# Performance work log

Hardware: AMD Instinct MI355X
Metric: run time of the kernel (lower is better)

## Reference

```python
import jax, jax.numpy as jnp
import numpy as np

K = 3        # kernel
S = 2        # downsample scale
P = 1        # padding
C = 96       # input channels
G = C // 6   # groups = 16 (use_group=True)
BN_EPS = 1e-5


def setup_inputs() -> dict:
    key = jax.random.key(0)
    k1, k2, k3, k4, k5 = jax.random.split(key, 5)
    b, h, w = 4, 256, 512
    x = jax.random.normal(k1, (b, C, h, w), dtype=jnp.float32)
    # convbn: Conv2d(C, C*S, k=3, stride=2, pad=1, bias=False) + BatchNorm2d(C*S)
    w1 = jax.random.normal(k2, (C * S, C, K, K), dtype=jnp.float32) * 0.05
    gamma = jax.random.uniform(k3, (C * S,), dtype=jnp.float32, minval=0.5, maxval=1.5)
    beta = jax.random.normal(k4, (C * S,), dtype=jnp.float32) * 0.1
    # 1x1 conv: C*S -> G * K^2, bias=False
    w2 = jax.random.normal(k5, (G * K * K, C * S, 1, 1), dtype=jnp.float32) * 0.05
    return {"x": x, "w1": w1, "gamma": gamma, "beta": beta, "w2": w2}


def _conv(x, w, stride, pad):
    return jax.lax.conv_general_dilated(
        x, w, window_strides=(stride, stride), padding=[(pad, pad), (pad, pad)],
        dimension_numbers=("NCHW", "OIHW", "NCHW"))


def _unfold_patches(x):
    # F.unfold(x, [K,K], stride=S, padding=P) viewed as (b, c, K*K, h', w')
    b, c, h, w = x.shape
    ho, wo = h // S, w // S
    xp = jnp.pad(x, ((0, 0), (0, 0), (P, P), (P, P)))
    taps = [xp[:, :, i:i + ho * S:S, j:j + wo * S:S] for i in range(K) for j in range(K)]
    return jnp.stack(taps, axis=2)  # (b, c, K^2, h', w')


def reference(x, w1, gamma, beta, w2):
    b, c, h, w = x.shape
    ho, wo = h // S, w // S
    # conv_mask branch: conv -> BN (eval: mean=0, var=1) -> LeakyReLU(0.1) -> 1x1 conv
    y = _conv(x, w1, S, P)
    y = y * (gamma / jnp.sqrt(1.0 + BN_EPS))[None, :, None, None] + beta[None, :, None, None]
    y = jnp.where(y >= 0, y, 0.1 * y)
    mask = _conv(y, w2, 1, 0)                                  # (b, G*K^2, h', w')
    mask = mask.reshape(b, 1, G, K * K, ho, wo)
    mask = jax.nn.softmax(mask, axis=3)
    # unfold and group split: channel index = i*G + g  (torch view semantics)
    patches = _unfold_patches(x)                               # (b, c, K^2, h', w')
    patches = patches.reshape(b, c // G, G, K * K, ho, wo)
    out = jnp.sum(mask * patches, axis=3)                      # (b, c//G, G, h', w')
    return out.reshape(b, c, ho, wo)
```

## Files before the change

kernel.cpp:

```cpp
#include <hip/hip_runtime.h>
#include <hip/hip_bf16.h>

#define Bb 4
#define Cc 96
#define Hh 256
#define Ww 512
#define OC 192
#define HO 128
#define WO 256
#define Gg 16
#define CPG 6

typedef __attribute__((ext_vector_type(4))) float f32x4;
typedef __attribute__((ext_vector_type(8))) short bf16x8;
typedef __attribute__((ext_vector_type(4))) short bf16x4;

static __device__ __forceinline__ ushort f2b(float f) {
    __hip_bfloat16 h = __float2bfloat16(f);
    return *reinterpret_cast<ushort*>(&h);
}
static __device__ __forceinline__ float b2f(ushort u) {
    unsigned int v = ((unsigned int)u) << 16;
    return __builtin_bit_cast(float, v);
}

__global__ __launch_bounds__(64) void pack_w1(const float* __restrict__ w1,
                                              ushort* __restrict__ apack) {
    const int blk = blockIdx.x;
    const int k0 = blk / 12;
    const int mf = blk % 12;
    const int lane = threadIdx.x;
    const int m = mf * 16 + (lane & 15);
    const int chunk = k0 / 9;
    const int tap = k0 % 9;
    ushort* dst = apack + (((size_t)(k0 * 12 + mf) * 64) + lane) * 8;
#pragma unroll
    for (int j = 0; j < 8; ++j) {
        const int klocal = ((lane >> 4) << 3) + j;
        const int ic = chunk * 32 + klocal;
        dst[j] = f2b(w1[(size_t)(m * Cc + ic) * 9 + tap]);
    }
}

__global__ __launch_bounds__(64) void pack_w2(const float* __restrict__ w2,
                                              ushort* __restrict__ w2p) {
    const int blk = blockIdx.x;
    const int ks = blk / 9;
    const int mf = blk % 9;
    const int lane = threadIdx.x;
    const int X = lane & 15;
    const int qq = X >> 2;
    const int rr = X & 3;
    const int s = mf * 4 + rr;
    const int g = qq * 4 + s / 9;
    const int k = s % 9;
    const int m = g * 9 + k;
    ushort* dst = w2p + (((size_t)(ks * 9 + mf) * 64) + lane) * 8;
#pragma unroll
    for (int j = 0; j < 8; ++j) {
        const int klocal = ((lane >> 4) << 3) + j;
        const int c = ks * 32 + klocal;
        dst[j] = f2b(w2[(size_t)m * OC + c]);
    }
}

#define XL_MAIN (6 * 4 * 128 * 8)
#define UNION_USHORTS (XL_MAIN + 3 * 32)

__global__ __launch_bounds__(512) void fused(
        const float* __restrict__ x, const ushort* __restrict__ apack,
        const ushort* __restrict__ w2p,
        const float* __restrict__ gamma, const float* __restrict__ beta,
        float* __restrict__ out) {
    __shared__ __align__(16) ushort smem[UNION_USHORTS];
    __shared__ float sc[OC], bi[OC];

    const int bid0 = blockIdx.x;
    const int bid = (bid0 & 7) * 128 + (bid0 >> 3);
    const int owt = bid & 1;
    const int oh = (bid >> 1) & 127;
    const int b = bid >> 8;
    const int ow0 = owt * 128;
    const int tid = threadIdx.x;
    const int wid = tid >> 6;
    const int wm = wid & 1;
    const int wn = wid >> 1;
    const int lane = tid & 63;
    const int r = lane & 15;
    const int q = lane >> 4;

    if (tid < OC) {
        const float bnr = 1.0f / sqrtf(1.0f + 1e-5f);
        sc[tid] = gamma[tid] * bnr;
        bi[tid] = beta[tid];
    }

    f32x4 cacc[6][2];
#pragma unroll
    for (int mf = 0; mf < 6; ++mf)
#pragma unroll
        for (int nf = 0; nf < 2; ++nf) cacc[mf][nf] = (f32x4){0.f, 0.f, 0.f, 0.f};

    const size_t chs = (size_t)Hh * Ww;

    for (int chunk = 0; chunk < 3; ++chunk) {
        __syncthreads();
        const int icc = chunk * 32;
#pragma unroll
        for (int it = 0; it < 3; ++it) {
            const int g2 = tid + (it << 9);
            const int oct = g2 & 3;
            const int colp = (g2 >> 2) & 127;
            const int row = g2 >> 9;
            const int ih = 2 * oh - 1 + row;
            const int gcol = 2 * ow0 + 2 * colp;
            float2 v[8];
            if (ih >= 0) {
                const float* xp = x + ((size_t)(b * Cc + icc + (oct << 3)) * Hh + ih) * Ww + gcol;
#pragma unroll
                for (int j = 0; j < 8; ++j)
                    v[j] = *reinterpret_cast<const float2*>(xp + (size_t)j * chs);
            } else {
#pragma unroll
                for (int j = 0; j < 8; ++j) v[j] = make_float2(0.f, 0.f);
            }
            bf16x8 u0, u1;
#pragma unroll
            for (int j = 0; j < 8; ++j) {
                u0[j] = (short)f2b(v[j].x);
                u1[j] = (short)f2b(v[j].y);
            }
            *reinterpret_cast<bf16x8*>(smem + (((row * 2 + 0) * 4 + oct) * 128 + colp) * 8) = u0;
            *reinterpret_cast<bf16x8*>(smem + (((row * 2 + 1) * 4 + oct) * 128 + colp) * 8) = u1;
        }
        if (tid < 12) {
            const int oct = tid & 3;
            const int row = tid >> 2;
            const int ih = 2 * oh - 1 + row;
            const int gcol = 2 * ow0 - 1;
            float v[8];
            if (ih >= 0 && gcol >= 0) {
                const float* xp = x + ((size_t)(b * Cc + icc + (oct << 3)) * Hh + ih) * Ww + gcol;
#pragma unroll
                for (int j = 0; j < 8; ++j) v[j] = xp[(size_t)j * chs];
            } else {
#pragma unroll
                for (int j = 0; j < 8; ++j) v[j] = 0.f;
            }
            bf16x8 u;
#pragma unroll
            for (int j = 0; j < 8; ++j) u[j] = (short)f2b(v[j]);
            *reinterpret_cast<bf16x8*>(smem + XL_MAIN + row * 32 + oct * 8) = u;
        }
        __syncthreads();

#pragma unroll
        for (int tap = 0; tap < 9; ++tap) {
            const int kh = tap / 3, kw = tap % 3;
            const int par = (kw == 1) ? 0 : 1;
            const int cb = (kw == 0) ? -1 : 0;
            const int k0 = chunk * 9 + tap;

            bf16x8 af[6];
            const ushort* ap = apack + (((size_t)(k0 * 12 + wm * 6) * 64) + lane) * 8;
#pragma unroll
            for (int mf = 0; mf < 6; ++mf)
                af[mf] = *reinterpret_cast<const bf16x8*>(ap + (size_t)mf * 64 * 8);

            bf16x8 bfr[2];
#pragma unroll
            for (int nf = 0; nf < 2; ++nf) {
                const int n = wn * 32 + nf * 16 + r;
                const int colc = n + cb;
                const ushort* src = (colc >= 0)
                    ? smem + (((kh * 2 + par) * 4 + q) * 128 + colc) * 8
                    : smem + XL_MAIN + kh * 32 + q * 8;
                bfr[nf] = *reinterpret_cast<const bf16x8*>(src);
            }
#pragma unroll
            for (int mf = 0; mf < 6; ++mf)
#pragma unroll
                for (int nf = 0; nf < 2; ++nf)
                    cacc[mf][nf] = __builtin_amdgcn_mfma_f32_16x16x32_bf16(
                        af[mf], bfr[nf], cacc[mf][nf], 0, 0, 0);
        }
    }

    __syncthreads();
#pragma unroll
    for (int mf = 0; mf < 6; ++mf) {
        const int cbase = wm * 96 + mf * 16;
        const int coct = (cbase >> 3) + (q >> 1);
#pragma unroll
        for (int nf = 0; nf < 2; ++nf) {
            const int ow = wn * 32 + nf * 16 + r;
            ushort pk[4];
#pragma unroll
            for (int rr = 0; rr < 4; ++rr) {
                const int oc = cbase + q * 4 + rr;
                float v = cacc[mf][nf][rr] * sc[oc] + bi[oc];
                v = (v >= 0.f) ? v : 0.1f * v;
                pk[rr] = f2b(v);
            }
            *reinterpret_cast<bf16x4*>(smem + (coct * 128 + ow) * 8 + (q & 1) * 4) =
                *reinterpret_cast<bf16x4*>(pk);
        }
    }
    __syncthreads();

    const int hi = wid >> 2;
    const int mfbase = hi * 4;
    f32x4 macc[5];
#pragma unroll
    for (int mf = 0; mf < 5; ++mf) macc[mf] = (f32x4){0.f, 0.f, 0.f, 0.f};

    const int owq = (wid & 3) * 32 + (q >> 1) * 16 + r;
    const int owq9 = (wid & 3) * 16 + r + ((wid >> 2) ? 0 : 0);
    (void)owq9;
#pragma unroll
    for (int ks = 0; ks < 6; ++ks) {
        bf16x8 af[5];
        const ushort* ap = w2p + (((size_t)(ks * 9 + mfbase) * 64) + lane) * 8;
#pragma unroll
        for (int mf = 0; mf < 5; ++mf)
            af[mf] = *reinterpret_cast<const bf16x8*>(ap + (size_t)mf * 64 * 8);
        bf16x8 bfr0 = *reinterpret_cast<const bf16x8*>(
            smem + ((ks * 4 + q) * 128 + (wid & 3) * 32 + 0 * 16 + r) * 8);
        bf16x8 bfr1 = *reinterpret_cast<const bf16x8*>(
            smem + ((ks * 4 + q) * 128 + (wid & 3) * 32 + 1 * 16 + r) * 8);
#pragma unroll
        for (int mf = 0; mf < 5; ++mf) {
            macc[mf] = __builtin_amdgcn_mfma_f32_16x16x32_bf16(af[mf], bfr0, macc[mf], 0, 0, 0);
        }
        (void)bfr1;
    }
    f32x4 macc2[5];
#pragma unroll
    for (int mf = 0; mf < 5; ++mf) macc2[mf] = (f32x4){0.f, 0.f, 0.f, 0.f};
#pragma unroll
    for (int ks = 0; ks < 6; ++ks) {
        bf16x8 af[5];
        const ushort* ap = w2p + (((size_t)(ks * 9 + mfbase) * 64) + lane) * 8;
#pragma unroll
        for (int mf = 0; mf < 5; ++mf)
            af[mf] = *reinterpret_cast<const bf16x8*>(ap + (size_t)mf * 64 * 8);
        bf16x8 bfr = *reinterpret_cast<const bf16x8*>(
            smem + ((ks * 4 + q) * 128 + (wid & 3) * 32 + 16 + r) * 8);
#pragma unroll
        for (int mf = 0; mf < 5; ++mf)
            macc2[mf] = __builtin_amdgcn_mfma_f32_16x16x32_bf16(af[mf], bfr, macc2[mf], 0, 0, 0);
    }
    __syncthreads();

#pragma unroll
    for (int nf = 0; nf < 2; ++nf) {
        const int ow = (wid & 3) * 32 + nf * 16 + r;
        const int col = (ow + q * 16) & 127;
#pragma unroll
        for (int gi = 0; gi < 2; ++gi) {
            const int gl = (wid >> 2) * 2 + gi;
            const int g = q * 4 + gl;
            float pv[9];
            float mx = -1e30f;
#pragma unroll
            for (int k = 0; k < 9; ++k) {
                const int s = gl * 9 + k;
                const int mi = (s >> 2) - ((wid >> 2) ? 4 : 0);
                pv[k] = 0.f; (void)mi;
            }
            (void)pv; (void)mx; (void)g; (void)col;
        }
        break;
    }
    {
        if (hi == 0) {
#pragma unroll
            for (int nf = 0; nf < 2; ++nf) {
                const int ow = (wid & 3) * 32 + nf * 16 + r;
                const int col = (ow + q * 16) & 127;
                const f32x4(&mc)[5] = (nf == 0) ? macc : macc2;
#pragma unroll
                for (int gi = 0; gi < 2; ++gi) {
                    const int gl = gi;
                    const int g = q * 4 + gl;
                    float pv[9]; float mx = -1e30f;
#pragma unroll
                    for (int k = 0; k < 9; ++k) {
                        const int s = gl * 9 + k;
                        pv[k] = mc[s >> 2][s & 3];
                        mx = fmaxf(mx, pv[k]);
                    }
                    float ssum = 0.f;
#pragma unroll
                    for (int k = 0; k < 9; ++k) { pv[k] = __expf(pv[k] - mx); ssum += pv[k]; }
                    const float inv = 1.f / ssum;
#pragma unroll
                    for (int k = 0; k < 9; ++k)
                        smem[(g * 9 + k) * 128 + col] = f2b(pv[k] * inv);
                }
            }
        } else {
#pragma unroll
            for (int nf = 0; nf < 2; ++nf) {
                const int ow = (wid & 3) * 32 + nf * 16 + r;
                const int col = (ow + q * 16) & 127;
                const f32x4(&mc)[5] = (nf == 0) ? macc : macc2;
#pragma unroll
                for (int gi = 0; gi < 2; ++gi) {
                    const int gl = 2 + gi;
                    const int g = q * 4 + gl;
                    float pv[9]; float mx = -1e30f;
#pragma unroll
                    for (int k = 0; k < 9; ++k) {
                        const int s = gl * 9 + k;
                        pv[k] = mc[(s >> 2) - 4][s & 3];
                        mx = fmaxf(mx, pv[k]);
                    }
                    float ssum = 0.f;
#pragma unroll
                    for (int k = 0; k < 9; ++k) { pv[k] = __expf(pv[k] - mx); ssum += pv[k]; }
                    const float inv = 1.f / ssum;
#pragma unroll
                    for (int k = 0; k < 9; ++k)
                        smem[(g * 9 + k) * 128 + col] = f2b(pv[k] * inv);
                }
            }
        }
    }
    __syncthreads();

    const int ih0 = 2 * oh - 1;
    const bool okh0 = (oh > 0);
#pragma unroll
    for (int it = 0; it < 4; ++it) {
        const int idx = (it << 9) + tid;
        const int g = idx >> 7;
        const int owl = idx & 127;
        const int owg = ow0 + owl;
        const int col = (owl + (g >> 2) * 16) & 127;

        float p[9];
#pragma unroll
        for (int k = 0; k < 9; ++k) p[k] = b2f(smem[(g * 9 + k) * 128 + col]);

        const int iw0 = 2 * owg - 1;
        const bool okw0 = (owg > 0);
#pragma unroll
        for (int i = 0; i < CPG; ++i) {
            const int cc = i * Gg + g;
            const float* xc = x + (size_t)(b * Cc + cc) * chs;
            float acc = 0.f;
#pragma unroll
            for (int kh = 0; kh < 3; ++kh) {
                if (kh == 0 && !okh0) continue;
                const float* rowp = xc + (size_t)(ih0 + kh) * Ww + iw0;
                const float v0 = okw0 ? rowp[0] : 0.f;
                const float2 v12 = *reinterpret_cast<const float2*>(rowp + 1);
                acc += p[kh * 3 + 0] * v0 + p[kh * 3 + 1] * v12.x
                     + p[kh * 3 + 2] * v12.y;
            }
            out[((size_t)(b * Cc + cc) * HO + oh) * WO + owg] = acc;
        }
    }
}

extern "C" void kernel_launch(void* const* d_in, const int* in_sizes, int n_in,
                              void* d_out, int out_size, void* d_ws, size_t ws_size,
                              hipStream_t stream) {
    const float* x     = (const float*)d_in[0];
    const float* w1    = (const float*)d_in[1];
    const float* gamma = (const float*)d_in[2];
    const float* beta  = (const float*)d_in[3];
    const float* w2    = (const float*)d_in[4];
    float* out = (float*)d_out;

    ushort* apack = (ushort*)d_ws;
    ushort* w2p   = (ushort*)((char*)d_ws + 331776);

    pack_w1<<<27 * 12, 64, 0, stream>>>(w1, apack);
    pack_w2<<<6 * 9, 64, 0, stream>>>(w2, w2p);
    fused<<<Bb * HO * 2, 512, 0, stream>>>(x, apack, w2p, gamma, beta, out);
}
```

Baseline: 174.6 us.

## Prefetch next input-channel chunk into registers during MFMA compute

Global loads of the next 32-channel input chunk are issued into registers right after the LDS barrier, so they overlap the conv MFMA taps of the current chunk instead of stalling at the start of each chunk. The two separate 1x1-conv MFMA loops are also merged so the w2 fragments are loaded once per k-step and feed both column halves. Launch bounds now request 4 blocks per CU. The extra prefetch registers (about 56 floats per thread) plus a tighter register cap could cause spills or reduce overlap.

```diff
diff --git a/kernel.cpp b/kernel.cpp
--- a/kernel.cpp
+++ b/kernel.cpp
@@ -67,7 +67,45 @@
 #define XL_MAIN (6 * 4 * 128 * 8)
 #define UNION_USHORTS (XL_MAIN + 3 * 32)
 
-__global__ __launch_bounds__(512) void fused(
+#define ISSUE_LOADS(CH)                                                        \
+    {                                                                          \
+        const int icc_ = (CH) * 32;                                            \
+        _Pragma("unroll")                                                      \
+        for (int it = 0; it < 3; ++it) {                                       \
+            const int g2 = tid + (it << 9);                                    \
+            const int oct = g2 & 3;                                            \
+            const int colp = (g2 >> 2) & 127;                                  \
+            const int row = g2 >> 9;                                           \
+            const int ih = 2 * oh - 1 + row;                                   \
+            const int gcol = 2 * ow0 + 2 * colp;                               \
+            float2* dst = (it == 0) ? pre0 : (it == 1) ? pre1 : pre2;          \
+            if (ih >= 0) {                                                     \
+                const float* xp = x + ((size_t)(b * Cc + icc_ + (oct << 3)) * Hh + ih) * Ww + gcol; \
+                _Pragma("unroll")                                              \
+                for (int j = 0; j < 8; ++j)                                    \
+                    dst[j] = *reinterpret_cast<const float2*>(xp + (size_t)j * chs); \
+            } else {                                                           \
+                _Pragma("unroll")                                              \
+                for (int j = 0; j < 8; ++j) dst[j] = make_float2(0.f, 0.f);    \
+            }                                                                  \
+        }                                                                      \
+        if (tid < 12) {                                                        \
+            const int oct = tid & 3;                                           \
+            const int row = tid >> 2;                                          \
+            const int ih = 2 * oh - 1 + row;                                   \
+            const int gcol = 2 * ow0 - 1;                                      \
+            if (ih >= 0 && gcol >= 0) {                                        \
+                const float* xp = x + ((size_t)(b * Cc + icc_ + (oct << 3)) * Hh + ih) * Ww + gcol; \
+                _Pragma("unroll")                                              \
+                for (int j = 0; j < 8; ++j) preh[j] = xp[(size_t)j * chs];     \
+            } else {                                                           \
+                _Pragma("unroll")                                              \
+                for (int j = 0; j < 8; ++j) preh[j] = 0.f;                     \
+            }                                                                  \
+        }                                                                      \
+    }
+
+__global__ __launch_bounds__(512, 4) void fused(
         const float* __restrict__ x, const ushort* __restrict__ apack,
         const ushort* __restrict__ w2p,
         const float* __restrict__ gamma, const float* __restrict__ beta,
@@ -103,32 +141,24 @@
 
     const size_t chs = (size_t)Hh * Ww;
 
+    float2 pre0[8], pre1[8], pre2[8];
+    float preh[8];
+
+    ISSUE_LOADS(0);
     for (int chunk = 0; chunk < 3; ++chunk) {
         __syncthreads();
-        const int icc = chunk * 32;
 #pragma unroll
         for (int it = 0; it < 3; ++it) {
             const int g2 = tid + (it << 9);
             const int oct = g2 & 3;
             const int colp = (g2 >> 2) & 127;
             const int row = g2 >> 9;
-            const int ih = 2 * oh - 1 + row;
-            const int gcol = 2 * ow0 + 2 * colp;
-            float2 v[8];
-            if (ih >= 0) {
-                const float* xp = x + ((size_t)(b * Cc + icc + (oct << 3)) * Hh + ih) * Ww + gcol;
-#pragma unroll
-                for (int j = 0; j < 8; ++j)
-                    v[j] = *reinterpret_cast<const float2*>(xp + (size_t)j * chs);
-            } else {
-#pragma unroll
-                for (int j = 0; j < 8; ++j) v[j] = make_float2(0.f, 0.f);
-            }
+            const float2* src = (it == 0) ? pre0 : (it == 1) ? pre1 : pre2;
             bf16x8 u0, u1;
 #pragma unroll
             for (int j = 0; j < 8; ++j) {
-                u0[j] = (short)f2b(v[j].x);
-                u1[j] = (short)f2b(v[j].y);
+                u0[j] = (short)f2b(src[j].x);
+                u1[j] = (short)f2b(src[j].y);
             }
             *reinterpret_cast<bf16x8*>(smem + (((row * 2 + 0) * 4 + oct) * 128 + colp) * 8) = u0;
             *reinterpret_cast<bf16x8*>(smem + (((row * 2 + 1) * 4 + oct) * 128 + colp) * 8) = u1;
@@ -136,23 +166,14 @@
         if (tid < 12) {
             const int oct = tid & 3;
             const int row = tid >> 2;
-            const int ih = 2 * oh - 1 + row;
-            const int gcol = 2 * ow0 - 1;
-            float v[8];
-            if (ih >= 0 && gcol >= 0) {
-                const float* xp = x + ((size_t)(b * Cc + icc + (oct << 3)) * Hh + ih) * Ww + gcol;
-#pragma unroll
-                for (int j = 0; j < 8; ++j) v[j] = xp[(size_t)j * chs];
-            } else {
-#pragma unroll
-                for (int j = 0; j < 8; ++j) v[j] = 0.f;
-            }
             bf16x8 u;
 #pragma unroll
-            for (int j = 0; j < 8; ++j) u[j] = (short)f2b(v[j]);
+            for (int j = 0; j < 8; ++j) u[j] = (short)f2b(preh[j]);
             *reinterpret_cast<bf16x8*>(smem + XL_MAIN + row * 32 + oct * 8) = u;
         }
         __syncthreads();
+        if (chunk == 0)      ISSUE_LOADS(1)
+        else if (chunk == 1) ISSUE_LOADS(2)
 
 #pragma unroll
         for (int tap = 0; tap < 9; ++tap) {
@@ -210,13 +231,12 @@
 
     const int hi = wid >> 2;
     const int mfbase = hi * 4;
-    f32x4 macc[5];
-#pragma unroll
-    for (int mf = 0; mf < 5; ++mf) macc[mf] = (f32x4){0.f, 0.f, 0.f, 0.f};
-
-    const int owq = (wid & 3) * 32 + (q >> 1) * 16 + r;
-    const int owq9 = (wid & 3) * 16 + r + ((wid >> 2) ? 0 : 0);
-    (void)owq9;
+    f32x4 macc[5], macc2[5];
+#pragma unroll
+    for (int mf = 0; mf < 5; ++mf) {
+        macc[mf] = (f32x4){0.f, 0.f, 0.f, 0.f};
+        macc2[mf] = (f32x4){0.f, 0.f, 0.f, 0.f};
+    }
 #pragma unroll
     for (int ks = 0; ks < 6; ++ks) {
         bf16x8 af[5];
@@ -224,106 +244,68 @@
 #pragma unroll
         for (int mf = 0; mf < 5; ++mf)
             af[mf] = *reinterpret_cast<const bf16x8*>(ap + (size_t)mf * 64 * 8);
-        bf16x8 bfr0 = *reinterpret_cast<const bf16x8*>(
-            smem + ((ks * 4 + q) * 128 + (wid & 3) * 32 + 0 * 16 + r) * 8);
-        bf16x8 bfr1 = *reinterpret_cast<const bf16x8*>(
-            smem + ((ks * 4 + q) * 128 + (wid & 3) * 32 + 1 * 16 + r) * 8);
+        const bf16x8 bfr0 = *reinterpret_cast<const bf16x8*>(
+            smem + ((ks * 4 + q) * 128 + (wid & 3) * 32 + r) * 8);
+        const bf16x8 bfr1 = *reinterpret_cast<const bf16x8*>(
+            smem + ((ks * 4 + q) * 128 + (wid & 3) * 32 + 16 + r) * 8);
 #pragma unroll
         for (int mf = 0; mf < 5; ++mf) {
             macc[mf] = __builtin_amdgcn_mfma_f32_16x16x32_bf16(af[mf], bfr0, macc[mf], 0, 0, 0);
-        }
-        (void)bfr1;
-    }
-    f32x4 macc2[5];
-#pragma unroll
-    for (int mf = 0; mf < 5; ++mf) macc2[mf] = (f32x4){0.f, 0.f, 0.f, 0.f};
-#pragma unroll
-    for (int ks = 0; ks < 6; ++ks) {
-        bf16x8 af[5];
-        const ushort* ap = w2p + (((size_t)(ks * 9 + mfbase) * 64) + lane) * 8;
-#pragma unroll
-        for (int mf = 0; mf < 5; ++mf)
-            af[mf] = *reinterpret_cast<const bf16x8*>(ap + (size_t)mf * 64 * 8);
-        bf16x8 bfr = *reinterpret_cast<const bf16x8*>(
-            smem + ((ks * 4 + q) * 128 + (wid & 3) * 32 + 16 + r) * 8);
-#pragma unroll
-        for (int mf = 0; mf < 5; ++mf)
-            macc2[mf] = __builtin_amdgcn_mfma_f32_16x16x32_bf16(af[mf], bfr, macc2[mf], 0, 0, 0);
+            macc2[mf] = __builtin_amdgcn_mfma_f32_16x16x32_bf16(af[mf], bfr1, macc2[mf], 0, 0, 0);
+        }
     }
     __syncthreads();
 
-#pragma unroll
-    for (int nf = 0; nf < 2; ++nf) {
-        const int ow = (wid & 3) * 32 + nf * 16 + r;
-        const int col = (ow + q * 16) & 127;
-#pragma unroll
-        for (int gi = 0; gi < 2; ++gi) {
-            const int gl = (wid >> 2) * 2 + gi;
-            const int g = q * 4 + gl;
-            float pv[9];
-            float mx = -1e30f;
-#pragma unroll
-            for (int k = 0; k < 9; ++k) {
-                const int s = gl * 9 + k;
-                const int mi = (s >> 2) - ((wid >> 2) ? 4 : 0);
-                pv[k] = 0.f; (void)mi;
-            }
-            (void)pv; (void)mx; (void)g; (void)col;
-        }
-        break;
-    }
-    {
-        if (hi == 0) {
-#pragma unroll
-            for (int nf = 0; nf < 2; ++nf) {
-                const int ow = (wid & 3) * 32 + nf * 16 + r;
-                const int col = (ow + q * 16) & 127;
-                const f32x4(&mc)[5] = (nf == 0) ? macc : macc2;
-#pragma unroll
-                for (int gi = 0; gi < 2; ++gi) {
-                    const int gl = gi;
-                    const int g = q * 4 + gl;
-                    float pv[9]; float mx = -1e30f;
-#pragma unroll
-                    for (int k = 0; k < 9; ++k) {
-                        const int s = gl * 9 + k;
-                        pv[k] = mc[s >> 2][s & 3];
-                        mx = fmaxf(mx, pv[k]);
-                    }
-                    float ssum = 0.f;
-#pragma unroll
-                    for (int k = 0; k < 9; ++k) { pv[k] = __expf(pv[k] - mx); ssum += pv[k]; }
-                    const float inv = 1.f / ssum;
-#pragma unroll
-                    for (int k = 0; k < 9; ++k)
-                        smem[(g * 9 + k) * 128 + col] = f2b(pv[k] * inv);
+    if (hi == 0) {
+#pragma unroll
+        for (int nf = 0; nf < 2; ++nf) {
+            const int ow = (wid & 3) * 32 + nf * 16 + r;
+            const int col = (ow + q * 16) & 127;
+            const f32x4(&mc)[5] = (nf == 0) ? macc : macc2;
+#pragma unroll
+            for (int gi = 0; gi < 2; ++gi) {
+                const int gl = gi;
+                const int g = q * 4 + gl;
+                float pv[9]; float mx = -1e30f;
+#pragma unroll
+                for (int k = 0; k < 9; ++k) {
+                    const int s = gl * 9 + k;
+                    pv[k] = mc[s >> 2][s & 3];
+                    mx = fmaxf(mx, pv[k]);
                 }
-            }
-        } else {
-#pragma unroll
-            for (int nf = 0; nf < 2; ++nf) {
-                const int ow = (wid & 3) * 32 + nf * 16 + r;
-                const int col = (ow + q * 16) & 127;
-                const f32x4(&mc)[5] = (nf == 0) ? macc : macc2;
-#pragma unroll
-                for (int gi = 0; gi < 2; ++gi) {
-                    const int gl = 2 + gi;
-                    const int g = q * 4 + gl;
-                    float pv[9]; float mx = -1e30f;
-#pragma unroll
-                    for (int k = 0; k < 9; ++k) {
-                        const int s = gl * 9 + k;
-                        pv[k] = mc[(s >> 2) - 4][s & 3];
-                        mx = fmaxf(mx, pv[k]);
-                    }
-                    float ssum = 0.f;
-#pragma unroll
-                    for (int k = 0; k < 9; ++k) { pv[k] = __expf(pv[k] - mx); ssum += pv[k]; }
-                    const float inv = 1.f / ssum;
-#pragma unroll
-                    for (int k = 0; k < 9; ++k)
-                        smem[(g * 9 + k) * 128 + col] = f2b(pv[k] * inv);
+                float ssum = 0.f;
+#pragma unroll
+                for (int k = 0; k < 9; ++k) { pv[k] = __expf(pv[k] - mx); ssum += pv[k]; }
+                const float inv = 1.f / ssum;
+#pragma unroll
+                for (int k = 0; k < 9; ++k)
+                    smem[(g * 9 + k) * 128 + col] = f2b(pv[k] * inv);
+            }
+        }
+    } else {
+#pragma unroll
+        for (int nf = 0; nf < 2; ++nf) {
+            const int ow = (wid & 3) * 32 + nf * 16 + r;
+            const int col = (ow + q * 16) & 127;
+            const f32x4(&mc)[5] = (nf == 0) ? macc : macc2;
+#pragma unroll
+            for (int gi = 0; gi < 2; ++gi) {
+                const int gl = 2 + gi;
+                const int g = q * 4 + gl;
+                float pv[9]; float mx = -1e30f;
+#pragma unroll
+                for (int k = 0; k < 9; ++k) {
+                    const int s = gl * 9 + k;
+                    pv[k] = mc[(s >> 2) - 4][s & 3];
+                    mx = fmaxf(mx, pv[k]);
                 }
+                float ssum = 0.f;
+#pragma unroll
+                for (int k = 0; k < 9; ++k) { pv[k] = __expf(pv[k] - mx); ssum += pv[k]; }
+                const float inv = 1.f / ssum;
+#pragma unroll
+                for (int k = 0; k < 9; ++k)
+                    smem[(g * 9 + k) * 128 + col] = f2b(pv[k] * inv);
             }
         }
     }
```

New measurement: 366.3 us. +109.8%, slower.
